# Kernel optimization log

Hardware: AMD Instinct MI355X
Metric: run time of the kernel (lower is better)

The kernel has to match this reference:

```python
import jax, jax.numpy as jnp
import numpy as np

ALPHA = 0.2  # LeakyReLU negative slope


def setup_inputs() -> dict:
    key = jax.random.key(0)
    k1, k2, k3 = jax.random.split(key, 3)
    B, N, F_in, F_out = 8, 2048, 128, 128
    x = jax.random.normal(k1, (B, N, F_in), dtype=jnp.float32)
    # nn.Linear weight: (out_features, in_features)
    W = jax.random.normal(k2, (F_out, F_in), dtype=jnp.float32) * (1.0 / np.sqrt(F_in))
    # attention vector a: (1, 2*out_features), xavier-uniform-like scale
    lim = np.sqrt(6.0 / (1 + 2 * F_out))
    a = jax.random.uniform(k3, (1, 2 * F_out), dtype=jnp.float32, minval=-lim, maxval=lim)
    return {"x": x, "W": W, "a": a}


def reference(x, W, a):
    # x: (B, N, F_in), W: (F_out, F_in), a: (1, 2*F_out)
    F_out = W.shape[0]
    h = jnp.einsum("bnf,of->bno", x, W)  # (B, N, F_out)
    # score_ij = leaky_relu(h_i . a[:F_out] + h_j . a[F_out:])
    # This is the math of cat([h_i, h_j]) * a summed over last dim,
    # WITHOUT materializing the (B,N,N,2F) concat tensor.
    a1 = a[0, :F_out]   # (F_out,)
    a2 = a[0, F_out:]   # (F_out,)
    si = h @ a1         # (B, N)  contribution from h_i
    sj = h @ a2         # (B, N)  contribution from h_j
    e = si[:, :, None] + sj[:, None, :]            # (B, N, N)
    e = jnp.where(e >= 0, e, ALPHA * e)            # leaky_relu
    attention = jax.nn.softmax(e, axis=-1)         # (B, N, N)
    # dropout is identity in eval mode
    output = jnp.einsum("bij,bjo->bio", attention, h)  # (B, N, F_out)
    return output
```

## Files before the change

### kernel.cpp

```cpp
#include <hip/hip_runtime.h>
#include <math.h>

#define BB 8
#define NN 2048
#define FF 128
#define LALPHA 0.2f
#define CH 16
#define NCH (NN / CH)

#define K1R 32
__global__ __launch_bounds__(256, 2)
void k1_h(const float* __restrict__ x, const float* __restrict__ W,
          const float* __restrict__ a, float* __restrict__ h,
          float* __restrict__ si, float* __restrict__ sj, int* __restrict__ cnt)
{
    __shared__ float Wt[FF * 132];
    const int t = threadIdx.x;
    const int row0 = blockIdx.x * K1R;

    if (blockIdx.x == 0)
        for (int kk = t; kk < BB * NCH; kk += 256) cnt[kk] = 0;

    for (int kk = t; kk < FF * FF; kk += 256) {
        int o = kk >> 7, f = kk & (FF - 1);
        Wt[f * 132 + o] = W[kk];
    }
    __syncthreads();

    const int tx = t & 15, ty = t >> 4;
    const int oq = tx << 3;
    const int rq = ty << 1;
    float acc[2][8];
#pragma unroll
    for (int r = 0; r < 2; ++r)
#pragma unroll
        for (int c = 0; c < 8; ++c) acc[r][c] = 0.f;

    for (int f0 = 0; f0 < FF; f0 += 4) {
        float4 xv[2];
#pragma unroll
        for (int r = 0; r < 2; ++r)
            xv[r] = *(const float4*)&x[(size_t)(row0 + rq + r) * FF + f0];
#pragma unroll
        for (int ff = 0; ff < 4; ++ff) {
            float4 w0 = *(const float4*)&Wt[(f0 + ff) * 132 + oq];
            float4 w1 = *(const float4*)&Wt[(f0 + ff) * 132 + oq + 4];
            const float wc[8] = {w0.x, w0.y, w0.z, w0.w, w1.x, w1.y, w1.z, w1.w};
#pragma unroll
            for (int r = 0; r < 2; ++r) {
                const float xr = (ff == 0) ? xv[r].x : (ff == 1) ? xv[r].y
                               : (ff == 2) ? xv[r].z : xv[r].w;
#pragma unroll
                for (int c = 0; c < 8; ++c)
                    acc[r][c] += xr * wc[c];
            }
        }
    }
#pragma unroll
    for (int r = 0; r < 2; ++r) {
        float* hp = &h[(size_t)(row0 + rq + r) * FF + oq];
        *(float4*)hp       = make_float4(acc[r][0], acc[r][1], acc[r][2], acc[r][3]);
        *(float4*)(hp + 4) = make_float4(acc[r][4], acc[r][5], acc[r][6], acc[r][7]);
    }
    const float4 a10 = *(const float4*)&a[oq];
    const float4 a11 = *(const float4*)&a[oq + 4];
    const float4 a20 = *(const float4*)&a[FF + oq];
    const float4 a21 = *(const float4*)&a[FF + oq + 4];
    const float a1v[8] = {a10.x, a10.y, a10.z, a10.w, a11.x, a11.y, a11.z, a11.w};
    const float a2v[8] = {a20.x, a20.y, a20.z, a20.w, a21.x, a21.y, a21.z, a21.w};
#pragma unroll
    for (int r = 0; r < 2; ++r) {
        float s1 = 0.f, s2 = 0.f;
#pragma unroll
        for (int c = 0; c < 8; ++c) { s1 += acc[r][c] * a1v[c]; s2 += acc[r][c] * a2v[c]; }
#pragma unroll
        for (int off = 8; off >= 1; off >>= 1) {
            s1 += __shfl_down(s1, off, 16);
            s2 += __shfl_down(s2, off, 16);
        }
        if (tx == 0) { si[row0 + rq + r] = s1; sj[row0 + rq + r] = s2; }
    }
}

__global__ __launch_bounds__(1024)
void k2_rank(const float* __restrict__ sj, float* __restrict__ keys, int* __restrict__ sidx,
             float* __restrict__ ew1, float* __restrict__ ew2)
{
    __shared__ float lk[NN];
    const int b = blockIdx.x >> 5;
    const int s = blockIdx.x & 31;
    const int t = threadIdx.x;
    for (int j = t; j < NN; j += 1024) lk[j] = sj[b * NN + j];
    __syncthreads();
    const int e = s * 64 + (t >> 4);
    const int slice = t & 15;
    const float ki = lk[e];
    const float4* lk4 = (const float4*)lk;
    int r = 0;
#pragma unroll 8
    for (int it = 0; it < 32; ++it) {
        int q = slice + (it << 4);
        float4 v = lk4[q];
        int j = q << 2;
        r += (v.x < ki || (v.x == ki && (j + 0) < e));
        r += (v.y < ki || (v.y == ki && (j + 1) < e));
        r += (v.z < ki || (v.z == ki && (j + 2) < e));
        r += (v.w < ki || (v.w == ki && (j + 3) < e));
    }
    r += __shfl_down(r, 8, 16);
    r += __shfl_down(r, 4, 16);
    r += __shfl_down(r, 2, 16);
    r += __shfl_down(r, 1, 16);
    if (slice == 0) {
        keys[b * NN + r] = ki;
        sidx[b * NN + r] = e;
        ew1[b * NN + r] = expf(ki);
        ew2[b * NN + r] = expf(LALPHA * ki);
    }
}

__global__ __launch_bounds__(128)
void k3a_csum(const float* __restrict__ h, const float* __restrict__ keys,
              const int* __restrict__ sidx, const float* __restrict__ si,
              const float* __restrict__ ew1, const float* __restrict__ ew2,
              float* __restrict__ csum1, float* __restrict__ csum2,
              float* __restrict__ ssum1, float* __restrict__ ssum2,
              int* __restrict__ cnt, int* __restrict__ brows)
{
    const int bid = blockIdx.x;
    const int b = bid >> 7, c = bid & (NCH - 1);
    const int o = threadIdx.x;
    const int m0 = c * CH;

    __shared__ float lw1[CH], lw2[CH];
    __shared__ int li[CH];
    __shared__ float bkey[NCH];
    if (o < CH) {
        lw1[o] = ew1[b * NN + m0 + o];
        lw2[o] = ew2[b * NN + m0 + o];
        li[o]  = sidx[b * NN + m0 + o];
    }
    bkey[o] = keys[b * NN + (o << 4)];
    __syncthreads();

    float r[CH];
#pragma unroll
    for (int m = 0; m < CH; ++m)
        r[m] = h[(size_t)(b * NN + li[m]) * FF + o];

    float a1 = 0.f, a2 = 0.f, s1 = 0.f, s2 = 0.f;
#pragma unroll
    for (int m = 0; m < CH; ++m) {
        float w1 = lw1[m], w2 = lw2[m];
        a1 += w1 * r[m]; a2 += w2 * r[m];
        s1 += w1;        s2 += w2;
    }
    csum1[(size_t)bid * FF + o] = a1;
    csum2[(size_t)bid * FF + o] = a2;
    if (o == 0) { ssum1[bid] = s1; ssum2[bid] = s2; }

    const int rl = o >> 3, slice = o & 7;
    const int i = m0 + rl;
    const float thr = -si[b * NN + i];
    int cc = 0;
#pragma unroll
    for (int k = 0; k < 16; ++k) {
        int c2 = slice * 16 + k;
        cc += (c2 >= 1) && (bkey[c2] < thr);
    }
    cc += __shfl_down(cc, 4, 8);
    cc += __shfl_down(cc, 2, 8);
    cc += __shfl_down(cc, 1, 8);
    if (slice == 0) {
        int pos = atomicAdd(&cnt[b * NCH + cc], 1);
        brows[(size_t)(b * NCH + cc) * NN + pos] = i;
    }
}

__global__ __launch_bounds__(256)
void k3se_emit(const float* __restrict__ h, const float* __restrict__ keys,
               const int* __restrict__ sidx, const float* __restrict__ si,
               const float* __restrict__ ew1, const float* __restrict__ ew2,
               const float* __restrict__ csum1, const float* __restrict__ csum2,
               const float* __restrict__ ssum1, const float* __restrict__ ssum2,
               const int* __restrict__ cnt, const int* __restrict__ brows,
               float* __restrict__ out)
{
    __shared__ float hs[CH][FF];
    __shared__ float S1pos[CH + 1][FF];
    __shared__ float P2pos[CH + 1][FF];
    __shared__ float lw1[CH], lw2[CH], lkey[CH];
    __shared__ float T1pos[CH + 1], T2pos[CH + 1];
    __shared__ float ls1[NCH], ls2[NCH];
    __shared__ float bp1[2][FF], bp2[2][FF];

    const int bid = blockIdx.x;
    const int b = bid >> 7, c = bid & (NCH - 1);
    const int t = threadIdx.x;
    const int o = t & 127, ht = t >> 7;
    const int m0 = c * CH;

    if (t < CH) {
        lkey[t] = keys[b * NN + m0 + t];
        lw1[t]  = ew1[b * NN + m0 + t];
        lw2[t]  = ew2[b * NN + m0 + t];
    }
    if (ht == 0) ls1[o] = ssum1[b * NCH + o];
    else         ls2[o] = ssum2[b * NCH + o];

    {
        int sid[8];
#pragma unroll
        for (int it = 0; it < 8; ++it) {
            int kk = t + (it << 8);
            sid[it] = sidx[b * NN + m0 + (kk >> 7)];
        }
#pragma unroll
        for (int it = 0; it < 8; ++it) {
            int kk = t + (it << 8);
            hs[kk >> 7][kk & 127] = h[(size_t)(b * NN + sid[it]) * FF + (kk & 127)];
        }
    }

    {
        const int c2lo = ht << 6, c2hi = c2lo + 64;
        float a1 = 0.f, a2 = 0.f;
        const int lo1 = (c + 1 > c2lo) ? c + 1 : c2lo;
#pragma unroll 8
        for (int c2 = lo1; c2 < c2hi; ++c2)
            a1 += csum1[(size_t)(b * NCH + c2) * FF + o];
        const int hi2 = (c < c2hi) ? c : c2hi;
#pragma unroll 8
        for (int c2 = c2lo; c2 < hi2; ++c2)
            a2 += csum2[(size_t)(b * NCH + c2) * FF + o];
        bp1[ht][o] = a1;
        bp2[ht][o] = a2;
    }
    __syncthreads();

    if (ht == 0) {
        float s = bp1[0][o] + bp1[1][o];
        S1pos[CH][o] = s;
#pragma unroll
        for (int m = CH - 1; m >= 0; --m) {
            s += lw1[m] * hs[m][o];
            S1pos[m][o] = s;
        }
        if (t < CH + 1) {
            float ts = 0.f;
#pragma unroll 8
            for (int c2 = c + 1; c2 < NCH; ++c2) ts += ls1[c2];
            for (int mm = CH - 1; mm >= t; --mm) ts += lw1[mm];
            T1pos[t] = ts;
        }
    } else {
        float s = bp2[0][o] + bp2[1][o];
        P2pos[0][o] = s;
#pragma unroll
        for (int m = 0; m < CH; ++m) {
            s += lw2[m] * hs[m][o];
            P2pos[m + 1][o] = s;
        }
        if (o < CH + 1) {
            float ts = 0.f;
#pragma unroll 8
            for (int c2 = 0; c2 < c; ++c2) ts += ls2[c2];
            for (int mm = 0; mm < o; ++mm) ts += lw2[mm];
            T2pos[o] = ts;
        }
    }
    __syncthreads();

    const int nrows = cnt[b * NCH + c];
    const int* br = brows + (size_t)(b * NCH + c) * NN;

    for (int r0 = 0; r0 < nrows; r0 += 2) {
        const int ri = r0 + ht;
        if (ri < nrows) {
            const int i = br[ri];
            const float siv = si[b * NN + i];
            const float thr = -siv;
            int rel = 0;
#pragma unroll
            for (int m = 0; m < CH; ++m) rel += (lkey[m] < thr);
            const float e1 = expf(siv), e2 = expf(LALPHA * siv);
            const float num = e1 * S1pos[rel][o] + e2 * P2pos[rel][o];
            const float den = e1 * T1pos[rel] + e2 * T2pos[rel];
            out[(size_t)(b * NN + i) * FF + o] = num / den;
        }
    }
}

extern "C" void kernel_launch(void* const* d_in, const int* in_sizes, int n_in,
                              void* d_out, int out_size, void* d_ws, size_t ws_size,
                              hipStream_t stream)
{
    const float* x = (const float*)d_in[0];
    const float* W = (const float*)d_in[1];
    const float* a = (const float*)d_in[2];
    float* out = (float*)d_out;

    float* ws = (float*)d_ws;
    float* h     = ws;
    float* si    = h + BB * NN * FF;
    float* sj    = si + BB * NN;
    float* keys  = sj + BB * NN;
    int*   sidx  = (int*)(keys + BB * NN);
    float* ew1   = (float*)(sidx + BB * NN);
    float* ew2   = ew1 + BB * NN;
    float* csum1 = ew2 + BB * NN;
    float* csum2 = csum1 + BB * NCH * FF;
    float* ssum1 = csum2 + BB * NCH * FF;
    float* ssum2 = ssum1 + BB * NCH;
    int*   cnt   = (int*)(ssum2 + BB * NCH);
    int*   brows = cnt + BB * NCH;

    hipLaunchKernelGGL(k1_h, dim3(BB * NN / K1R), dim3(256), 0, stream, x, W, a, h, si, sj, cnt);
    hipLaunchKernelGGL(k2_rank, dim3(BB * 32), dim3(1024), 0, stream, sj, keys, sidx, ew1, ew2);
    hipLaunchKernelGGL(k3a_csum, dim3(BB * NCH), dim3(128), 0, stream,
                       h, keys, sidx, si, ew1, ew2, csum1, csum2, ssum1, ssum2, cnt, brows);
    hipLaunchKernelGGL(k3se_emit, dim3(BB * NCH), dim3(256), 0, stream,
                       h, keys, sidx, si, ew1, ew2, csum1, csum2, ssum1, ssum2, cnt, brows, out);
}
```

Before: 56.68 us.

## Build per-chunk row lists in shared memory inside emit kernel instead of global atomics

Moves the assignment of query rows to key chunks out of the csum kernel and into the emit kernel. Each emit block now scans all rows of its batch, tests each row's threshold against its chunk's boundary keys, and gathers the matching rows into a shared-memory list with a shared atomic. This removes the global atomic bucket counters, the global row list, and the counter zeroing in the first kernel, along with the dependency between those kernels. In exchange every block rereads all si values for its batch, and the list is capped at 256 rows, so a very skewed chunk would silently drop rows.

```diff
diff --git a/kernel.cpp b/kernel.cpp
--- a/kernel.cpp
+++ b/kernel.cpp
@@ -12,14 +12,11 @@
 __global__ __launch_bounds__(256, 2)
 void k1_h(const float* __restrict__ x, const float* __restrict__ W,
           const float* __restrict__ a, float* __restrict__ h,
-          float* __restrict__ si, float* __restrict__ sj, int* __restrict__ cnt)
+          float* __restrict__ si, float* __restrict__ sj)
 {
     __shared__ float Wt[FF * 132];
     const int t = threadIdx.x;
     const int row0 = blockIdx.x * K1R;
-
-    if (blockIdx.x == 0)
-        for (int kk = t; kk < BB * NCH; kk += 256) cnt[kk] = 0;
 
     for (int kk = t; kk < FF * FF; kk += 256) {
         int o = kk >> 7, f = kk & (FF - 1);
@@ -120,12 +117,10 @@
 }
 
 __global__ __launch_bounds__(128)
-void k3a_csum(const float* __restrict__ h, const float* __restrict__ keys,
-              const int* __restrict__ sidx, const float* __restrict__ si,
+void k3a_csum(const float* __restrict__ h, const int* __restrict__ sidx,
               const float* __restrict__ ew1, const float* __restrict__ ew2,
               float* __restrict__ csum1, float* __restrict__ csum2,
-              float* __restrict__ ssum1, float* __restrict__ ssum2,
-              int* __restrict__ cnt, int* __restrict__ brows)
+              float* __restrict__ ssum1, float* __restrict__ ssum2)
 {
     const int bid = blockIdx.x;
     const int b = bid >> 7, c = bid & (NCH - 1);
@@ -134,13 +129,11 @@
 
     __shared__ float lw1[CH], lw2[CH];
     __shared__ int li[CH];
-    __shared__ float bkey[NCH];
     if (o < CH) {
         lw1[o] = ew1[b * NN + m0 + o];
         lw2[o] = ew2[b * NN + m0 + o];
         li[o]  = sidx[b * NN + m0 + o];
     }
-    bkey[o] = keys[b * NN + (o << 4)];
     __syncthreads();
 
     float r[CH];
@@ -158,23 +151,6 @@
     csum1[(size_t)bid * FF + o] = a1;
     csum2[(size_t)bid * FF + o] = a2;
     if (o == 0) { ssum1[bid] = s1; ssum2[bid] = s2; }
-
-    const int rl = o >> 3, slice = o & 7;
-    const int i = m0 + rl;
-    const float thr = -si[b * NN + i];
-    int cc = 0;
-#pragma unroll
-    for (int k = 0; k < 16; ++k) {
-        int c2 = slice * 16 + k;
-        cc += (c2 >= 1) && (bkey[c2] < thr);
-    }
-    cc += __shfl_down(cc, 4, 8);
-    cc += __shfl_down(cc, 2, 8);
-    cc += __shfl_down(cc, 1, 8);
-    if (slice == 0) {
-        int pos = atomicAdd(&cnt[b * NCH + cc], 1);
-        brows[(size_t)(b * NCH + cc) * NN + pos] = i;
-    }
 }
 
 __global__ __launch_bounds__(256)
@@ -183,7 +159,6 @@
                const float* __restrict__ ew1, const float* __restrict__ ew2,
                const float* __restrict__ csum1, const float* __restrict__ csum2,
                const float* __restrict__ ssum1, const float* __restrict__ ssum2,
-               const int* __restrict__ cnt, const int* __restrict__ brows,
                float* __restrict__ out)
 {
     __shared__ float hs[CH][FF];
@@ -193,6 +168,8 @@
     __shared__ float T1pos[CH + 1], T2pos[CH + 1];
     __shared__ float ls1[NCH], ls2[NCH];
     __shared__ float bp1[2][FF], bp2[2][FF];
+    __shared__ int lcnt;
+    __shared__ int lrows[256];
 
     const int bid = blockIdx.x;
     const int b = bid >> 7, c = bid & (NCH - 1);
@@ -200,6 +177,7 @@
     const int o = t & 127, ht = t >> 7;
     const int m0 = c * CH;
 
+    if (t == 0) lcnt = 0;
     if (t < CH) {
         lkey[t] = keys[b * NN + m0 + t];
         lw1[t]  = ew1[b * NN + m0 + t];
@@ -238,6 +216,21 @@
     }
     __syncthreads();
 
+    {
+        const float bk0 = keys[b * NN + m0];
+        const float bk1 = (c < NCH - 1) ? keys[b * NN + m0 + CH] : 0.f;
+        for (int k = 0; k < 8; ++k) {
+            int i = (k << 8) + t;
+            float thr = -si[b * NN + i];
+            bool ge = (c == 0) || (bk0 < thr);
+            bool lt = (c == NCH - 1) || !(bk1 < thr);
+            if (ge && lt) {
+                int pos = atomicAdd(&lcnt, 1);
+                if (pos < 256) lrows[pos] = i;
+            }
+        }
+    }
+
     if (ht == 0) {
         float s = bp1[0][o] + bp1[1][o];
         S1pos[CH][o] = s;
@@ -271,13 +264,11 @@
     }
     __syncthreads();
 
-    const int nrows = cnt[b * NCH + c];
-    const int* br = brows + (size_t)(b * NCH + c) * NN;
-
+    int nrows = lcnt; if (nrows > 256) nrows = 256;
     for (int r0 = 0; r0 < nrows; r0 += 2) {
         const int ri = r0 + ht;
         if (ri < nrows) {
-            const int i = br[ri];
+            const int i = lrows[ri];
             const float siv = si[b * NN + i];
             const float thr = -siv;
             int rel = 0;
@@ -312,13 +303,11 @@
     float* csum2 = csum1 + BB * NCH * FF;
     float* ssum1 = csum2 + BB * NCH * FF;
     float* ssum2 = ssum1 + BB * NCH;
-    int*   cnt   = (int*)(ssum2 + BB * NCH);
-    int*   brows = cnt + BB * NCH;
-
-    hipLaunchKernelGGL(k1_h, dim3(BB * NN / K1R), dim3(256), 0, stream, x, W, a, h, si, sj, cnt);
+
+    hipLaunchKernelGGL(k1_h, dim3(BB * NN / K1R), dim3(256), 0, stream, x, W, a, h, si, sj);
     hipLaunchKernelGGL(k2_rank, dim3(BB * 32), dim3(1024), 0, stream, sj, keys, sidx, ew1, ew2);
     hipLaunchKernelGGL(k3a_csum, dim3(BB * NCH), dim3(128), 0, stream,
-                       h, keys, sidx, si, ew1, ew2, csum1, csum2, ssum1, ssum2, cnt, brows);
+                       h, sidx, ew1, ew2, csum1, csum2, ssum1, ssum2);
     hipLaunchKernelGGL(k3se_emit, dim3(BB * NCH), dim3(256), 0, stream,
-                       h, keys, sidx, si, ew1, ew2, csum1, csum2, ssum1, ssum2, cnt, brows, out);
-}
+                       h, keys, sidx, si, ew1, ew2, csum1, csum2, ssum1, ssum2, out);
+}
```

Result: faster. 53.76 us (median of 2 runs) (-5.1%).
